# Performance work log

Hardware: AMD Instinct MI355X
Metric: run time of the kernel (lower is better)

## Reference

```python
import jax, jax.numpy as jnp
import numpy as np

IN_SIZE, Q_SIZE, V_SIZE = 1024, 128, 1024
B, S = 8, 2048


def setup_inputs() -> dict:
    key = jax.random.key(0)
    ks = jax.random.split(key, 7)
    scale = 1.0 / np.sqrt(IN_SIZE)
    x = jax.random.normal(ks[0], (B, S, IN_SIZE), dtype=jnp.float32)
    Wq = jax.random.uniform(ks[1], (IN_SIZE, Q_SIZE), dtype=jnp.float32, minval=-scale, maxval=scale)
    bq = jax.random.uniform(ks[2], (Q_SIZE,), dtype=jnp.float32, minval=-scale, maxval=scale)
    Wk = jax.random.uniform(ks[3], (IN_SIZE, Q_SIZE), dtype=jnp.float32, minval=-scale, maxval=scale)
    bk = jax.random.uniform(ks[4], (Q_SIZE,), dtype=jnp.float32, minval=-scale, maxval=scale)
    Wv = jax.random.uniform(ks[5], (IN_SIZE, V_SIZE), dtype=jnp.float32, minval=-scale, maxval=scale)
    bv = jax.random.uniform(ks[6], (V_SIZE,), dtype=jnp.float32, minval=-scale, maxval=scale)
    return {"x": x, "Wq": Wq, "bq": bq, "Wk": Wk, "bk": bk, "Wv": Wv, "bv": bv}


def reference(x, Wq, bq, Wk, bk, Wv, bv):
    # Projections: [B, S, q_size] / [B, S, v_size]
    q = jnp.einsum('bsi,iq->bsq', x, Wq) + bq
    k = jnp.einsum('bsi,iq->bsq', x, Wk) + bk
    v = jnp.einsum('bsi,iv->bsv', x, Wv) + bv
    # Unscaled attention scores [B, S, S] (module has no 1/sqrt(d) scale)
    scores = jnp.einsum('bsq,btq->bst', q, k)
    attn = jax.nn.softmax(scores, axis=-1)
    out = jnp.einsum('bst,btv->bsv', attn, v)
    return jnp.tanh(out)
```

## Files before the change

kernel.cpp:

```cpp
#include <hip/hip_runtime.h>
#include <hip/hip_bf16.h>
#include <stdint.h>

#define BM 128
#define BN 128
#define BK 64

typedef __attribute__((ext_vector_type(8))) short    bf16x8;
typedef __attribute__((ext_vector_type(8))) _Float16 f16x8;
typedef __attribute__((ext_vector_type(4))) float    f32x4;

typedef __attribute__((address_space(1))) void GV;
typedef __attribute__((address_space(3))) void LV;

__device__ __forceinline__ unsigned short f2bf(float f){
  union { float f; unsigned u; } x; x.f = f;
  unsigned r = x.u + 0x7fffu + ((x.u >> 16) & 1u);
  return (unsigned short)(r >> 16);
}
__device__ __forceinline__ float bf2f(unsigned short h){
  union { unsigned u; float f; } x; x.u = ((unsigned)h) << 16; return x.f;
}
__device__ __forceinline__ unsigned short f2h(float f){
  union { _Float16 h; unsigned short u; } c; c.h = (_Float16)f; return c.u;
}


__device__ __forceinline__ void stage_tile(const unsigned short* __restrict__ src, int ld,
                                           unsigned short* lds, int tid){
  #pragma unroll
  for (int t = 0; t < 4; ++t){
    int idx = t*256 + tid;
    int row = idx >> 3;
    int kc  = (idx & 7) ^ (row & 7);
    const unsigned short* g = src + (size_t)row*ld + kc*8;
    __builtin_amdgcn_global_load_lds((GV*)g, (LV*)(lds + idx*8), 16, 0, 0);
  }
}

__device__ __forceinline__ bf16x8 frag_ld(const unsigned short* lds, int r, int k){
  int byte = ((r << 7) + (k << 1)) ^ ((r & 7) << 4);
  return *(const bf16x8*)((const char*)lds + byte);
}

template<bool F16>
__device__ __forceinline__ void gemm_core(const unsigned short* __restrict__ At,
                                          const unsigned short* __restrict__ Bt,
                                          int lda, int ldb, int nkt,
                                          unsigned short* lsA, unsigned short* lsB,
                                          f32x4 (&acc)[4][4]){
  const int tid  = threadIdx.x;
  const int lane = tid & 63;
  const int wr = ((tid >> 7) & 1) << 6;
  const int wc = ((tid >> 6) & 1) << 6;
  const int l15 = lane & 15, lg = lane >> 4;

  for (int kt = 0; kt < nkt; ++kt){
    stage_tile(At + (size_t)kt*BK, lda, lsA, tid);
    stage_tile(Bt + (size_t)kt*BK, ldb, lsB, tid);
    __syncthreads();
    #pragma unroll
    for (int kk = 0; kk < 2; ++kk){
      bf16x8 af[4], bfr[4];
      #pragma unroll
      for (int mf = 0; mf < 4; ++mf) af[mf]  = frag_ld(lsA, wr + mf*16 + l15, kk*32 + lg*8);
      #pragma unroll
      for (int nf = 0; nf < 4; ++nf) bfr[nf] = frag_ld(lsB, wc + nf*16 + l15, kk*32 + lg*8);
      #pragma unroll
      for (int mf = 0; mf < 4; ++mf)
        #pragma unroll
        for (int nf = 0; nf < 4; ++nf){
          if constexpr (F16)
            acc[mf][nf] = __builtin_amdgcn_mfma_f32_16x16x32_f16(
                __builtin_bit_cast(f16x8, af[mf]), __builtin_bit_cast(f16x8, bfr[nf]),
                acc[mf][nf], 0, 0, 0);
          else
            acc[mf][nf] = __builtin_amdgcn_mfma_f32_16x16x32_bf16(af[mf], bfr[nf], acc[mf][nf], 0, 0, 0);
        }
    }
    __syncthreads();
  }
}

#define ZERO_ACC(acc) { _Pragma("unroll") for (int i_=0;i_<4;++i_) _Pragma("unroll") for (int j_=0;j_<4;++j_) acc[i_][j_] = (f32x4){0.f,0.f,0.f,0.f}; }

__global__ __launch_bounds__(256) void k_cvt_x(const float* __restrict__ x,
                                               unsigned short* __restrict__ xh, int n4){
  int i = blockIdx.x*blockDim.x + threadIdx.x;
  int stride = gridDim.x*blockDim.x;
  for (; i < n4; i += stride){
    float4 v = ((const float4*)x)[i];
    ushort4 o; o.x = f2h(v.x); o.y = f2h(v.y); o.z = f2h(v.z); o.w = f2h(v.w);
    ((ushort4*)xh)[i] = o;
  }
}

__global__ __launch_bounds__(256) void k_cvt_wt(const float* __restrict__ Wq, const float* __restrict__ Wk,
                                                const float* __restrict__ Wv, unsigned short* __restrict__ Wt){
  int n = blockIdx.x*32 + threadIdx.x;
  int k = blockIdx.y*8  + threadIdx.y;
  float v;
  if (n < 128)      v = Wq[(size_t)k*128  + n];
  else if (n < 256) v = Wk[(size_t)k*128  + (n-128)];
  else              v = Wv[(size_t)k*1024 + (n-256)];
  Wt[(size_t)n*1024 + k] = f2h(v);
}

__global__ __launch_bounds__(256) void k_proj(const unsigned short* __restrict__ xh,
                                              const unsigned short* __restrict__ Wt,
                                              const float* __restrict__ bq, const float* __restrict__ bk,
                                              const float* __restrict__ bv,
                                              unsigned short* __restrict__ Qh, unsigned short* __restrict__ Kh,
                                              unsigned short* __restrict__ Vt){
  __shared__ unsigned short lsA[BM*BK], lsB[BN*BK];
  const int m0 = blockIdx.x * BM;
  const int n0 = blockIdx.y * BN;
  f32x4 acc[4][4]; ZERO_ACC(acc);
  gemm_core<true>(xh + (size_t)m0*1024, Wt + (size_t)n0*1024, 1024, 1024, 16, lsA, lsB, acc);

  const int tid = threadIdx.x, lane = tid & 63;
  const int wr = ((tid >> 7) & 1) << 6;
  const int wc = ((tid >> 6) & 1) << 6;
  const int l15 = lane & 15, lg = lane >> 4;

  if (n0 < 256){
    unsigned short* T   = (n0 == 0) ? Qh : Kh;
    const float*  bias  = (n0 == 0) ? bq : bk;
    #pragma unroll
    for (int mf = 0; mf < 4; ++mf){
      #pragma unroll
      for (int nf = 0; nf < 4; ++nf){
        int c = wc + nf*16 + l15;
        float bi = bias[c];
        #pragma unroll
        for (int r = 0; r < 4; ++r){
          int gr = m0 + wr + mf*16 + lg*4 + r;
          T[(size_t)gr*128 + c] = f2h(acc[mf][nf][r] + bi);
        }
      }
    }
  } else {
    int jb = n0 - 256;
    #pragma unroll
    for (int mf = 0; mf < 4; ++mf){
      int gr0 = m0 + wr + mf*16 + lg*4;
      int b   = gr0 >> 11;
      int t0  = gr0 & 2047;
      #pragma unroll
      for (int nf = 0; nf < 4; ++nf){
        int j = jb + wc + nf*16 + l15;
        float bi = bv[j];
        ushort4 pk;
        pk.x = f2bf(acc[mf][nf][0] + bi);
        pk.y = f2bf(acc[mf][nf][1] + bi);
        pk.z = f2bf(acc[mf][nf][2] + bi);
        pk.w = f2bf(acc[mf][nf][3] + bi);
        *(ushort4*)(Vt + ((size_t)b*1024 + j)*2048 + t0) = pk;
      }
    }
  }
}

__global__ __launch_bounds__(256) void k_scores(const unsigned short* __restrict__ Qh,
                                                const unsigned short* __restrict__ Kh,
                                                unsigned short* __restrict__ P, float* __restrict__ lsum){
  __shared__ unsigned short lsA[BM*BK], lsB[BN*BK];
  const int s0 = blockIdx.x * BM;
  const int t0 = blockIdx.y * BN;
  const int b  = blockIdx.z;
  f32x4 acc[4][4]; ZERO_ACC(acc);
  gemm_core<true>(Qh + ((size_t)b*2048 + s0)*128, Kh + ((size_t)b*2048 + t0)*128, 128, 128, 2, lsA, lsB, acc);

  unsigned short* Pb = P + (size_t)b*2048*2048;
  float* lb = lsum + b*2048;
  const int tid = threadIdx.x, lane = tid & 63;
  const int wr = ((tid >> 7) & 1) << 6;
  const int wc = ((tid >> 6) & 1) << 6;
  const int l15 = lane & 15, lg = lane >> 4;

  #pragma unroll
  for (int mf = 0; mf < 4; ++mf){
    #pragma unroll
    for (int r = 0; r < 4; ++r){
      int sr = s0 + wr + mf*16 + lg*4 + r;
      float rsum = 0.f;
      #pragma unroll
      for (int nf = 0; nf < 4; ++nf){
        float e = __expf(acc[mf][nf][r]);
        unsigned short h = f2bf(e);
        int tc = t0 + wc + nf*16 + l15;
        Pb[(size_t)sr*2048 + tc] = h;
        rsum += bf2f(h);
      }
      #pragma unroll
      for (int d = 1; d < 16; d <<= 1) rsum += __shfl_xor(rsum, d);
      if (l15 == 0) atomicAdd(&lb[sr], rsum);
    }
  }
}

__global__ __launch_bounds__(256) void k_pv(const unsigned short* __restrict__ P,
                                            const unsigned short* __restrict__ Vt,
                                            const float* __restrict__ lsum, float* __restrict__ out){
  __shared__ unsigned short lsA[BM*BK], lsB[BN*BK];
  const int s0 = blockIdx.x * BM;
  const int j0 = blockIdx.y * BN;
  const int b  = blockIdx.z;
  f32x4 acc[4][4]; ZERO_ACC(acc);
  gemm_core<false>(P  + ((size_t)b*2048 + s0)*2048,
                   Vt + ((size_t)b*1024 + j0)*2048, 2048, 2048, 32, lsA, lsB, acc);

  const float* lb = lsum + b*2048;
  float* ob = out + (size_t)b*2048*1024;
  const int tid = threadIdx.x, lane = tid & 63;
  const int wr = ((tid >> 7) & 1) << 6;
  const int wc = ((tid >> 6) & 1) << 6;
  const int l15 = lane & 15, lg = lane >> 4;

  #pragma unroll
  for (int mf = 0; mf < 4; ++mf){
    #pragma unroll
    for (int r = 0; r < 4; ++r){
      int sr = s0 + wr + mf*16 + lg*4 + r;
      float rl = 1.0f / lb[sr];
      #pragma unroll
      for (int nf = 0; nf < 4; ++nf){
        int jc = j0 + wc + nf*16 + l15;
        float v = acc[mf][nf][r] * rl;
        ob[(size_t)sr*1024 + jc] = 1.0f - 2.0f/(1.0f + __expf(2.0f*v));
      }
    }
  }
}

extern "C" void kernel_launch(void* const* d_in, const int* in_sizes, int n_in,
                              void* d_out, int out_size, void* d_ws, size_t ws_size,
                              hipStream_t stream){
  const float* x  = (const float*)d_in[0];
  const float* Wq = (const float*)d_in[1];
  const float* bq = (const float*)d_in[2];
  const float* Wk = (const float*)d_in[3];
  const float* bk = (const float*)d_in[4];
  const float* Wv = (const float*)d_in[5];
  const float* bv = (const float*)d_in[6];
  float* out = (float*)d_out;

  char* ws = (char*)d_ws;
  const size_t MB = 1024*1024;
  unsigned short* Wt   = (unsigned short*)(ws);
  unsigned short* Qh   = (unsigned short*)(ws + 4*MB);
  unsigned short* Kh   = (unsigned short*)(ws + 8*MB);
  unsigned short* Vt   = (unsigned short*)(ws + 12*MB);
  unsigned short* P    = (unsigned short*)(ws + 44*MB);
  float*          lsum = (float*)(ws + 108*MB);
  unsigned short* xh   = (unsigned short*)d_out;

  hipMemsetAsync(lsum, 0, 16384*sizeof(float), stream);
  k_cvt_x  <<<2048, 256, 0, stream>>>(x, xh, 16384*1024/4);
  k_cvt_wt <<<dim3(40,128), dim3(32,8), 0, stream>>>(Wq, Wk, Wv, Wt);
  k_proj   <<<dim3(128,10), 256, 0, stream>>>(xh, Wt, bq, bk, bv, Qh, Kh, Vt);
  k_scores <<<dim3(16,16,8), 256, 0, stream>>>(Qh, Kh, P, lsum);
  k_pv     <<<dim3(16,8,8),  256, 0, stream>>>(P, Vt, lsum, out);
}
```

Baseline: 237.0 us.

## Replace PV GEMM with 256x256-tile, 8-wave, double-buffered pipelined kernel

The P·V GEMM moves from a 128x128 tile with 4 waves and a synchronous stage-then-compute loop to a 256x256 tile with 8 waves. LDS is double-buffered, with async global-to-LDS loads of the next K tile interleaved with MFMA phases, explicit waitcnt and barriers, and raised priority around the MFMA blocks. The goal is to hide load latency and increase operand reuse per tile. It uses 128KB of dynamic shared memory, which relies on the hardware allowing that much LDS per block. The grid drops to 256 blocks, which may underfill the GPU's compute units.

```diff
diff --git a/kernel.cpp b/kernel.cpp
--- a/kernel.cpp
+++ b/kernel.cpp
@@ -25,6 +25,10 @@
   union { _Float16 h; unsigned short u; } c; c.h = (_Float16)f; return c.u;
 }
 
+__device__ __forceinline__ bf16x8 frag_ld(const unsigned short* lds, int r, int k){
+  int byte = ((r << 7) + (k << 1)) ^ ((r & 7) << 4);
+  return *(const bf16x8*)((const char*)lds + byte);
+}
 
 __device__ __forceinline__ void stage_tile(const unsigned short* __restrict__ src, int ld,
                                            unsigned short* lds, int tid){
@@ -36,11 +40,6 @@
     const unsigned short* g = src + (size_t)row*ld + kc*8;
     __builtin_amdgcn_global_load_lds((GV*)g, (LV*)(lds + idx*8), 16, 0, 0);
   }
-}
-
-__device__ __forceinline__ bf16x8 frag_ld(const unsigned short* lds, int r, int k){
-  int byte = ((r << 7) + (k << 1)) ^ ((r & 7) << 4);
-  return *(const bf16x8*)((const char*)lds + byte);
 }
 
 template<bool F16>
@@ -199,33 +198,147 @@
   }
 }
 
-__global__ __launch_bounds__(256) void k_pv(const unsigned short* __restrict__ P,
-                                            const unsigned short* __restrict__ Vt,
-                                            const float* __restrict__ lsum, float* __restrict__ out){
-  __shared__ unsigned short lsA[BM*BK], lsB[BN*BK];
-  const int s0 = blockIdx.x * BM;
-  const int j0 = blockIdx.y * BN;
-  const int b  = blockIdx.z;
-  f32x4 acc[4][4]; ZERO_ACC(acc);
-  gemm_core<false>(P  + ((size_t)b*2048 + s0)*2048,
-                   Vt + ((size_t)b*1024 + j0)*2048, 2048, 2048, 32, lsA, lsB, acc);
+
+#define SBAR() { __builtin_amdgcn_sched_barrier(0); __builtin_amdgcn_s_barrier(); __builtin_amdgcn_sched_barrier(0); }
+#define LGKM0() { asm volatile("s_waitcnt lgkmcnt(0)" ::: "memory"); __builtin_amdgcn_sched_barrier(0); }
+
+__device__ __forceinline__ void stage_rows(const unsigned short* __restrict__ src, int ld,
+                                           unsigned short* lds, int row0, int tid){
+  #pragma unroll
+  for (int q = 0; q < 2; ++q){
+    int i  = q*512 + tid;
+    int lr = i >> 3;
+    int r  = row0 + lr;
+    int kc = (i & 7) ^ (r & 7);
+    __builtin_amdgcn_global_load_lds((GV*)(src + (size_t)r*ld + kc*8),
+                                     (LV*)(lds + (size_t)row0*64 + i*8), 16, 0, 0);
+  }
+}
+
+__global__ __launch_bounds__(512, 2) void k_pv8(const unsigned short* __restrict__ P,
+                                                const unsigned short* __restrict__ Vt,
+                                                const float* __restrict__ lsum,
+                                                float* __restrict__ out){
+  extern __shared__ unsigned short sm[];
+
+  const int tid  = threadIdx.x;
+  const int lane = tid & 63, l15 = lane & 15, lg = lane >> 4;
+  const int wid  = tid >> 6;
+  const int wrow0 = (wid >> 2) << 7;
+  const int wcol0 = (wid & 3) << 6;
+
+  const int bid = blockIdx.x;
+  const int b   = bid & 7;
+  const int r2  = bid >> 3;
+  const int s0  = (r2 >> 2) << 8;
+  const int j0  = (r2 & 3) << 8;
+
+  const unsigned short* Abase = P  + ((size_t)b*2048 + s0)*2048;
+  const unsigned short* Bbase = Vt + ((size_t)b*1024 + j0)*2048;
+  const int nkt = 32;
+
+  f32x4 acc[8][4];
+  #pragma unroll
+  for (int i = 0; i < 8; ++i)
+    #pragma unroll
+    for (int j = 0; j < 4; ++j) acc[i][j] = (f32x4){0.f,0.f,0.f,0.f};
+
+  {
+    unsigned short* A0 = sm;             unsigned short* B0 = sm + 32768;
+    unsigned short* B1 = sm + 49152;
+    stage_rows(Abase,      2048, A0, 0,   tid);
+    stage_rows(Abase,      2048, A0, 128, tid);
+    stage_rows(Bbase,      2048, B0, 0,   tid);
+    stage_rows(Bbase,      2048, B0, 128, tid);
+    stage_rows(Bbase + 64, 2048, B1, 0,   tid);
+    stage_rows(Bbase + 64, 2048, B1, 128, tid);
+  }
+  asm volatile("s_waitcnt vmcnt(4)" ::: "memory");
+  __builtin_amdgcn_sched_barrier(0);
+  SBAR();
+
+  for (int t = 0; t < nkt; ++t){
+    unsigned short* A  = sm + ((t & 1) << 14);
+    unsigned short* B  = sm + 32768 + ((t & 1) << 14);
+    unsigned short* An = sm + (((t + 1) & 1) << 14);
+    bf16x8 af[4], bfr[4];
+
+    #pragma unroll
+    for (int mf = 0; mf < 4; ++mf) af[mf]  = frag_ld(A, wrow0 + mf*16 + l15, lg*8);
+    #pragma unroll
+    for (int nf = 0; nf < 4; ++nf) bfr[nf] = frag_ld(B, wcol0 + nf*16 + l15, lg*8);
+    if (t + 1 < nkt) stage_rows(Abase + (size_t)(t+1)*64, 2048, An, 0, tid);
+    SBAR(); LGKM0();
+    __builtin_amdgcn_s_setprio(1);
+    #pragma unroll
+    for (int mf = 0; mf < 4; ++mf)
+      #pragma unroll
+      for (int nf = 0; nf < 4; ++nf)
+        acc[mf][nf] = __builtin_amdgcn_mfma_f32_16x16x32_bf16(af[mf], bfr[nf], acc[mf][nf], 0, 0, 0);
+    __builtin_amdgcn_s_setprio(0);
+    SBAR();
+
+    #pragma unroll
+    for (int mf = 0; mf < 4; ++mf) af[mf] = frag_ld(A, wrow0 + (mf+4)*16 + l15, lg*8);
+    if (t + 1 < nkt) stage_rows(Abase + (size_t)(t+1)*64, 2048, An, 128, tid);
+    SBAR(); LGKM0();
+    __builtin_amdgcn_s_setprio(1);
+    #pragma unroll
+    for (int mf = 0; mf < 4; ++mf)
+      #pragma unroll
+      for (int nf = 0; nf < 4; ++nf)
+        acc[mf+4][nf] = __builtin_amdgcn_mfma_f32_16x16x32_bf16(af[mf], bfr[nf], acc[mf+4][nf], 0, 0, 0);
+    __builtin_amdgcn_s_setprio(0);
+    SBAR();
+
+    #pragma unroll
+    for (int mf = 0; mf < 4; ++mf) af[mf]  = frag_ld(A, wrow0 + mf*16 + l15, 32 + lg*8);
+    #pragma unroll
+    for (int nf = 0; nf < 4; ++nf) bfr[nf] = frag_ld(B, wcol0 + nf*16 + l15, 32 + lg*8);
+    SBAR(); LGKM0();
+    __builtin_amdgcn_s_setprio(1);
+    #pragma unroll
+    for (int mf = 0; mf < 4; ++mf)
+      #pragma unroll
+      for (int nf = 0; nf < 4; ++nf)
+        acc[mf][nf] = __builtin_amdgcn_mfma_f32_16x16x32_bf16(af[mf], bfr[nf], acc[mf][nf], 0, 0, 0);
+    __builtin_amdgcn_s_setprio(0);
+    SBAR();
+
+    #pragma unroll
+    for (int mf = 0; mf < 4; ++mf) af[mf] = frag_ld(A, wrow0 + (mf+4)*16 + l15, 32 + lg*8);
+    if (t + 2 < nkt){
+      stage_rows(Bbase + (size_t)(t+2)*64, 2048, B, 0,   tid);
+      stage_rows(Bbase + (size_t)(t+2)*64, 2048, B, 128, tid);
+      asm volatile("s_waitcnt vmcnt(4)" ::: "memory");
+      __builtin_amdgcn_sched_barrier(0);
+    } else if (t + 1 < nkt){
+      asm volatile("s_waitcnt vmcnt(0)" ::: "memory");
+      __builtin_amdgcn_sched_barrier(0);
+    }
+    SBAR(); LGKM0();
+    __builtin_amdgcn_s_setprio(1);
+    #pragma unroll
+    for (int mf = 0; mf < 4; ++mf)
+      #pragma unroll
+      for (int nf = 0; nf < 4; ++nf)
+        acc[mf+4][nf] = __builtin_amdgcn_mfma_f32_16x16x32_bf16(af[mf], bfr[nf], acc[mf+4][nf], 0, 0, 0);
+    __builtin_amdgcn_s_setprio(0);
+    SBAR();
+  }
 
   const float* lb = lsum + b*2048;
   float* ob = out + (size_t)b*2048*1024;
-  const int tid = threadIdx.x, lane = tid & 63;
-  const int wr = ((tid >> 7) & 1) << 6;
-  const int wc = ((tid >> 6) & 1) << 6;
-  const int l15 = lane & 15, lg = lane >> 4;
-
-  #pragma unroll
-  for (int mf = 0; mf < 4; ++mf){
+  #pragma unroll
+  for (int mf = 0; mf < 8; ++mf){
     #pragma unroll
     for (int r = 0; r < 4; ++r){
-      int sr = s0 + wr + mf*16 + lg*4 + r;
+      int srl = wrow0 + mf*16 + lg*4 + r;
+      int sr  = s0 + srl;
       float rl = 1.0f / lb[sr];
       #pragma unroll
       for (int nf = 0; nf < 4; ++nf){
-        int jc = j0 + wc + nf*16 + l15;
+        int jc = j0 + wcol0 + nf*16 + l15;
         float v = acc[mf][nf][r] * rl;
         ob[(size_t)sr*1024 + jc] = 1.0f - 2.0f/(1.0f + __expf(2.0f*v));
       }
@@ -260,5 +373,5 @@
   k_cvt_wt <<<dim3(40,128), dim3(32,8), 0, stream>>>(Wq, Wk, Wv, Wt);
   k_proj   <<<dim3(128,10), 256, 0, stream>>>(xh, Wt, bq, bk, bv, Qh, Kh, Vt);
   k_scores <<<dim3(16,16,8), 256, 0, stream>>>(Qh, Kh, P, lsum);
-  k_pv     <<<dim3(16,8,8),  256, 0, stream>>>(P, Vt, lsum, out);
-}
+  k_pv8    <<<256, 512, 131072, stream>>>(P, Vt, lsum, out);
+}
```

After: 213.0 us. 1.11x faster.
